# Performance work log

Hardware: AMD Instinct MI355X
Metric: run time of the kernel (lower is better)

## Reference

```python
import jax, jax.numpy as jnp
import numpy as np
import math

B, N, DIM = 4, 2048, 512
HEADS, DIM_HEAD = 8, 64
INNER = HEADS * DIM_HEAD  # 512


def setup_inputs() -> dict:
    key = jax.random.key(0)
    ks = jax.random.split(key, 4)
    x = jax.random.normal(ks[0], (B, N, DIM), dtype=jnp.float32)
    # nn.Linear(dim, inner*4, bias=False): store as [dim, 4*inner] for x @ W
    w_qkvg = jax.random.normal(ks[1], (DIM, 4 * INNER), dtype=jnp.float32) * (1.0 / math.sqrt(DIM))
    sigma = jnp.full((1, HEADS, 1, 1), 1.92, dtype=jnp.float32)
    w_out = jax.random.normal(ks[2], (2 * INNER, DIM), dtype=jnp.float32) * (1.0 / math.sqrt(2 * INNER))
    b_out = jax.random.normal(ks[3], (DIM,), dtype=jnp.float32) * 0.01
    return {"x": x, "w_qkvg": w_qkvg, "sigma": sigma, "w_out": w_out, "b_out": b_out}


def reference(x, w_qkvg, sigma, w_out, b_out):
    b, n, d = x.shape
    h, dh = HEADS, DIM_HEAD
    scale = dh ** (-0.5)

    qkvg = x @ w_qkvg  # [b, n, 4*inner]
    q, k, vg, vsigma = jnp.split(qkvg, 4, axis=-1)

    def to_heads(t):  # [b, n, h*dh] -> [b, h, n, dh]
        return t.reshape(b, n, h, dh).transpose(0, 2, 1, 3)

    q, k, vg, vsigma = map(to_heads, (q, k, vg, vsigma))

    # --- softmax branch ---
    dots = jnp.einsum('bhid,bhjd->bhij', q, k) * scale  # [b, h, n, n]
    corr_g = jax.nn.softmax(dots, axis=-1)
    out_g = jnp.matmul(corr_g, vg)  # [b, h, n, dh]

    # --- Gaussian positional-mask branch ---
    pos = jnp.arange(1, n + 1, dtype=x.dtype)
    diffs = jnp.abs(pos[:, None] - pos[None, :])  # [n, n]
    inv_norm = 1.0 / (jnp.sqrt(jnp.asarray(2.0 * math.pi, x.dtype)) * sigma)  # [1, h, 1, 1]
    gm = inv_norm * jnp.exp(-(diffs ** 2)[None, None] / (2.0 * sigma ** 2))  # [1, h, n, n]
    corr_sigma = gm / gm.sum(-1, keepdims=True)
    out_s = jnp.matmul(corr_sigma, vsigma)  # broadcasts over batch -> [b, h, n, dh]

    out = jnp.concatenate([out_g, out_s], axis=-1)  # [b, h, n, 2*dh]
    out = out.transpose(0, 2, 1, 3).reshape(b, n, 2 * h * dh)
    return out @ w_out + b_out
```

## Files before the change

### kernel.cpp

```cpp
#include <hip/hip_runtime.h>

typedef _Float16 f16;
typedef __attribute__((ext_vector_type(8))) _Float16 f16x8;
typedef __attribute__((ext_vector_type(4))) _Float16 f16x4;
typedef __attribute__((ext_vector_type(4))) float f32x4;

#define B_ 4
#define N_ 2048
#define DIM_ 512
#define H_ 8
#define DH_ 64

__device__ __forceinline__ void gload16(const void* g, void* l) {
    __builtin_amdgcn_global_load_lds((const __attribute__((address_space(1))) void*)g,
                                     (__attribute__((address_space(3))) void*)l, 16, 0, 0);
}


__global__ __launch_bounds__(256) void cvt_f16_k8(const float* __restrict__ in,
                                                  f16* __restrict__ out, int n8) {
    int i = blockIdx.x * 256 + threadIdx.x;
    if (i < n8) {
        const float4 a = ((const float4*)in)[i * 2];
        const float4 b = ((const float4*)in)[i * 2 + 1];
        f16x8 o = {(f16)a.x, (f16)a.y, (f16)a.z, (f16)a.w,
                   (f16)b.x, (f16)b.y, (f16)b.z, (f16)b.w};
        ((f16x8*)out)[i] = o;
    }
}

__global__ __launch_bounds__(256) void transpose_cvt_k(const float* __restrict__ in,
                                                       f16* __restrict__ out, int K, int N) {
    __shared__ f16 tile[64][72];
    const int nbk = K >> 6;
    const int bk = blockIdx.x % nbk, bn = blockIdx.x / nbk;
    const int k0 = bk << 6, n0 = bn << 6;
    const int t = threadIdx.x;
    const int r = t >> 2, q = (t & 3) << 4;
#pragma unroll
    for (int u = 0; u < 4; u++) {
        const float4 v = *(const float4*)&in[(size_t)(k0 + r) * N + n0 + q + u * 4];
        tile[q + u * 4 + 0][r] = (f16)v.x;
        tile[q + u * 4 + 1][r] = (f16)v.y;
        tile[q + u * 4 + 2][r] = (f16)v.z;
        tile[q + u * 4 + 3][r] = (f16)v.w;
    }
    __syncthreads();
#pragma unroll
    for (int u = 0; u < 2; u++) {
        f16x8 o = *(const f16x8*)&tile[r][q + u * 8];
        *(f16x8*)&out[(size_t)(n0 + r) * K + k0 + q + u * 8] = o;
    }
}

template <int EPI>
__global__ __launch_bounds__(256) void gemm_bt(
    const f16* __restrict__ A, const f16* __restrict__ BT, int K, int N,
    f16* __restrict__ qb, f16* __restrict__ kb, f16* __restrict__ vbT,
    float* __restrict__ vsb, const float* __restrict__ bias, float* __restrict__ outp)
{
    __shared__ char sAb[16384];
    __shared__ char sBb[16384];
    const int tid = threadIdx.x;
    const int m0 = blockIdx.y * 128, n0 = blockIdx.x * 128;
    const int wave = tid >> 6, lane = tid & 63;
    const int wr = wave >> 1, wc = wave & 1;
    const int lr = lane & 15, lg = lane >> 4;

    f32x4 acc[4][4];
    const f32x4 zero = {0.f, 0.f, 0.f, 0.f};
#pragma unroll
    for (int i = 0; i < 4; i++)
#pragma unroll
        for (int j = 0; j < 4; j++) acc[i][j] = zero;

    const f16* srcA[4]; const f16* srcB[4];
    char* ldsA[4]; char* ldsB[4];
#pragma unroll
    for (int u = 0; u < 4; u++) {
        int row = wave * 8 + u * 32 + (lane >> 3);
        int e0 = ((lane & 7) ^ (row & 7)) << 3;
        srcA[u] = A + (size_t)(m0 + row) * K + e0;
        srcB[u] = BT + (size_t)(n0 + row) * K + e0;
        ldsA[u] = sAb + wave * 1024 + u * 4096;
        ldsB[u] = sBb + wave * 1024 + u * 4096;
    }

    const int swz = (lr & 7) << 4;
    for (int kt = 0; kt < K; kt += 64) {
#pragma unroll
        for (int u = 0; u < 4; u++) {
            gload16(srcA[u], ldsA[u]);
            gload16(srcB[u], ldsB[u]);
            srcA[u] += 64; srcB[u] += 64;
        }
        __syncthreads();
#pragma unroll
        for (int half = 0; half < 2; half++) {
            f16x8 af[4], bf[4];
#pragma unroll
            for (int i = 0; i < 4; i++) {
                int R = wr * 64 + i * 16 + lr;
                af[i] = *(const f16x8*)(sAb + R * 128 + (((half << 6) | (lg << 4)) ^ swz));
            }
#pragma unroll
            for (int j = 0; j < 4; j++) {
                int R = wc * 64 + j * 16 + lr;
                bf[j] = *(const f16x8*)(sBb + R * 128 + (((half << 6) | (lg << 4)) ^ swz));
            }
#pragma unroll
            for (int i = 0; i < 4; i++)
#pragma unroll
                for (int j = 0; j < 4; j++)
                    acc[i][j] = __builtin_amdgcn_mfma_f32_16x16x32_f16(af[i], bf[j], acc[i][j], 0, 0, 0);
        }
        __syncthreads();
    }

#pragma unroll
    for (int i = 0; i < 4; i++) {
#pragma unroll
        for (int j = 0; j < 4; j++) {
            int col = n0 + wc * 64 + j * 16 + lr;
            int row0 = m0 + wr * 64 + i * 16 + lg * 4;
            if (EPI == 0) {
                int sec = col >> 9, cc = col & 511;
                int h = cc >> 6, d = cc & 63;
                int b = row0 >> 11, ns = row0 & 2047;
                if (sec == 2) {
                    f16x4 o;
#pragma unroll
                    for (int r = 0; r < 4; r++) o[r] = (f16)acc[i][j][r];
                    *(f16x4*)&vbT[((size_t)(b * H_ + h) * DH_ + d) * N_ + ns] = o;
                } else if (sec == 0) {
#pragma unroll
                    for (int r = 0; r < 4; r++)
                        qb[((size_t)(b * H_ + h) * N_ + ns + r) * DH_ + d] = (f16)(acc[i][j][r] * 0.1803368801f);
                } else if (sec == 1) {
#pragma unroll
                    for (int r = 0; r < 4; r++)
                        kb[((size_t)(b * H_ + h) * N_ + ns + r) * DH_ + d] = (f16)acc[i][j][r];
                } else {
#pragma unroll
                    for (int r = 0; r < 4; r++)
                        vsb[((size_t)(b * H_ + h) * N_ + ns + r) * DH_ + d] = acc[i][j][r];
                }
            } else {
#pragma unroll
                for (int r = 0; r < 4; r++)
                    outp[(size_t)(row0 + r) * N + col] = acc[i][j][r] + bias[col];
            }
        }
    }
}

__global__ __launch_bounds__(256) void gemm_small(
    const f16* __restrict__ A, const f16* __restrict__ BT, int K, int N,
    const float* __restrict__ bias, float* __restrict__ outp)
{
    __shared__ char sAb[8192];
    __shared__ char sBb[8192];
    const int tid = threadIdx.x;
    const int m0 = blockIdx.y * 64, n0 = blockIdx.x * 64;
    const int wave = tid >> 6, lane = tid & 63;
    const int wr = wave >> 1, wc = wave & 1;
    const int lr = lane & 15, lg = lane >> 4;

    f32x4 acc[2][2];
    const f32x4 zero = {0.f, 0.f, 0.f, 0.f};
#pragma unroll
    for (int i = 0; i < 2; i++)
#pragma unroll
        for (int j = 0; j < 2; j++) acc[i][j] = zero;

    const f16* srcA[2]; const f16* srcB[2];
    char* ldsA[2]; char* ldsB[2];
#pragma unroll
    for (int u = 0; u < 2; u++) {
        int row = wave * 8 + u * 32 + (lane >> 3);
        int e0 = ((lane & 7) ^ (row & 7)) << 3;
        srcA[u] = A + (size_t)(m0 + row) * K + e0;
        srcB[u] = BT + (size_t)(n0 + row) * K + e0;
        ldsA[u] = sAb + wave * 1024 + u * 4096;
        ldsB[u] = sBb + wave * 1024 + u * 4096;
    }

    const int swz = (lr & 7) << 4;
    for (int kt = 0; kt < K; kt += 64) {
#pragma unroll
        for (int u = 0; u < 2; u++) {
            gload16(srcA[u], ldsA[u]);
            gload16(srcB[u], ldsB[u]);
            srcA[u] += 64; srcB[u] += 64;
        }
        __syncthreads();
#pragma unroll
        for (int half = 0; half < 2; half++) {
            f16x8 af[2], bf[2];
#pragma unroll
            for (int i = 0; i < 2; i++) {
                int R = wr * 32 + i * 16 + lr;
                af[i] = *(const f16x8*)(sAb + R * 128 + (((half << 6) | (lg << 4)) ^ swz));
            }
#pragma unroll
            for (int j = 0; j < 2; j++) {
                int R = wc * 32 + j * 16 + lr;
                bf[j] = *(const f16x8*)(sBb + R * 128 + (((half << 6) | (lg << 4)) ^ swz));
            }
#pragma unroll
            for (int i = 0; i < 2; i++)
#pragma unroll
                for (int j = 0; j < 2; j++)
                    acc[i][j] = __builtin_amdgcn_mfma_f32_16x16x32_f16(af[i], bf[j], acc[i][j], 0, 0, 0);
        }
        __syncthreads();
    }

#pragma unroll
    for (int i = 0; i < 2; i++)
#pragma unroll
        for (int j = 0; j < 2; j++) {
            int col = n0 + wc * 32 + j * 16 + lr;
            int row0 = m0 + wr * 32 + i * 16 + lg * 4;
#pragma unroll
            for (int r = 0; r < 4; r++)
                outp[(size_t)(row0 + r) * N + col] = acc[i][j][r] + bias[col];
        }
}

__global__ __launch_bounds__(256) void attn_k(
    const f16* __restrict__ qb, const f16* __restrict__ kb, const f16* __restrict__ vbT,
    f16* __restrict__ cat)
{
    __shared__ char sKbf[3 * 8192];
    __shared__ char sVbf[2 * 8192];
    const int tid = threadIdx.x;
    const int bid0 = blockIdx.x;
    const int obid = (bid0 & 7) * 64 + (bid0 >> 3);
    const int bh = obid >> 4, qblk = obid & 15;
    const int b = bh >> 3, h = bh & 7;
    const int wave = tid >> 6, lane = tid & 63;
    const int lr = lane & 15, lg = lane >> 4;

    const size_t base = (size_t)bh * N_ * DH_;
    const int qrow_a = qblk * 128 + wave * 32 + lr;
    const int qrow_b = qrow_a + 16;
    const f16x8 qfa0 = *(const f16x8*)&qb[base + (size_t)qrow_a * DH_ + lg * 8];
    const f16x8 qfa1 = *(const f16x8*)&qb[base + (size_t)qrow_a * DH_ + 32 + lg * 8];
    const f16x8 qfb0 = *(const f16x8*)&qb[base + (size_t)qrow_b * DH_ + lg * 8];
    const f16x8 qfb1 = *(const f16x8*)&qb[base + (size_t)qrow_b * DH_ + 32 + lg * 8];

    const f16* kq[2]; const f16* vq[2];
#pragma unroll
    for (int u = 0; u < 2; u++) {
        int row = wave * 8 + u * 32 + (lane >> 3);
        int e0 = ((lane & 7) ^ (row & 7)) << 3;
        kq[u] = kb + base + (size_t)row * 64 + e0;
        vq[u] = vbT + base + (size_t)row * 2048 + e0;
    }
    char* const ldsKw = sKbf + wave * 1024;
    char* const ldsVw = sVbf + wave * 1024;

    f32x4 Ota[4], Otb[4], lacc_a, lacc_b;
    const f32x4 zero = {0.f, 0.f, 0.f, 0.f};
#pragma unroll
    for (int dt = 0; dt < 4; dt++) { Ota[dt] = zero; Otb[dt] = zero; }
    lacc_a = zero; lacc_b = zero;
    const f16x4 onesA = {(f16)1.f, (f16)1.f, (f16)1.f, (f16)1.f};

    const int swz = (lr & 7) << 4;

#pragma unroll
    for (int u = 0; u < 2; u++) gload16(kq[u], ldsKw + u * 4096);
#pragma unroll
    for (int u = 0; u < 2; u++) gload16(vq[u], ldsVw + u * 4096);
#pragma unroll
    for (int u = 0; u < 2; u++) gload16(kq[u] + 4096, ldsKw + 8192 + u * 4096);

    int kcur = 0;
    int kpre = 2;
    for (int t = 0; t < 32; t++) {
        __builtin_amdgcn_s_barrier();
        {
            const int vtn = (t + 1) & 31, ktn = (t + 2) & 31;
            char* vdst = ldsVw + ((t + 1) & 1) * 8192;
            char* kdst = ldsKw + kpre * 8192;
#pragma unroll
            for (int u = 0; u < 2; u++) gload16(vq[u] + vtn * 64, vdst + u * 4096);
#pragma unroll
            for (int u = 0; u < 2; u++) gload16(kq[u] + ktn * 4096, kdst + u * 4096);
        }
        asm volatile("s_waitcnt vmcnt(6)" ::: "memory");
        __builtin_amdgcn_sched_barrier(0);

        const char* Kb = sKbf + kcur * 8192;
        const char* Vb = sVbf + (t & 1) * 8192;

        f32x4 sta[4], stb[4];
        __builtin_amdgcn_s_setprio(1);
#pragma unroll
        for (int ct = 0; ct < 4; ct++) {
            int row = ct * 16 + lr;
            f16x8 kf0 = *(const f16x8*)(Kb + (((row << 7) | (lg << 4)) ^ swz));
            f16x8 kf1 = *(const f16x8*)(Kb + (((row << 7) | 64 | (lg << 4)) ^ swz));
            f32x4 sa = __builtin_amdgcn_mfma_f32_16x16x32_f16(kf0, qfa0, zero, 0, 0, 0);
            sta[ct]  = __builtin_amdgcn_mfma_f32_16x16x32_f16(kf1, qfa1, sa, 0, 0, 0);
            f32x4 sb = __builtin_amdgcn_mfma_f32_16x16x32_f16(kf0, qfb0, zero, 0, 0, 0);
            stb[ct]  = __builtin_amdgcn_mfma_f32_16x16x32_f16(kf1, qfb1, sb, 0, 0, 0);
        }
        __builtin_amdgcn_s_setprio(0);

        f16x4 ppa[4], ppb[4];
#pragma unroll
        for (int ct = 0; ct < 4; ct++)
#pragma unroll
            for (int r = 0; r < 4; r++) {
                ppa[ct][r] = (f16)__builtin_amdgcn_exp2f(sta[ct][r]);
                ppb[ct][r] = (f16)__builtin_amdgcn_exp2f(stb[ct][r]);
            }

        __builtin_amdgcn_s_setprio(1);
#pragma unroll
        for (int ct = 0; ct < 4; ct++) {
            lacc_a = __builtin_amdgcn_mfma_f32_16x16x16f16(onesA, ppa[ct], lacc_a, 0, 0, 0);
            lacc_b = __builtin_amdgcn_mfma_f32_16x16x16f16(onesA, ppb[ct], lacc_b, 0, 0, 0);
        }
#pragma unroll
        for (int dt = 0; dt < 4; dt++) {
            int row = dt * 16 + lr;
#pragma unroll
            for (int ct = 0; ct < 4; ct++) {
                f16x4 vt = *(const f16x4*)(Vb + (((row << 7) | (ct * 32) | (lg << 3)) ^ swz));
                Ota[dt] = __builtin_amdgcn_mfma_f32_16x16x16f16(vt, ppa[ct], Ota[dt], 0, 0, 0);
                Otb[dt] = __builtin_amdgcn_mfma_f32_16x16x16f16(vt, ppb[ct], Otb[dt], 0, 0, 0);
            }
        }
        __builtin_amdgcn_s_setprio(0);

        kcur = (kcur == 2) ? 0 : kcur + 1;
        kpre = (kpre == 2) ? 0 : kpre + 1;
    }

    float inv_a = 1.0f / lacc_a[0];
    float inv_b = 1.0f / lacc_b[0];
#pragma unroll
    for (int dt = 0; dt < 4; dt++) {
        f16x4 oa, ob;
#pragma unroll
        for (int r = 0; r < 4; r++) {
            oa[r] = (f16)(Ota[dt][r] * inv_a);
            ob[r] = (f16)(Otb[dt][r] * inv_b);
        }
        *(f16x4*)&cat[((size_t)(b * N_ + qrow_a)) * 1024 + h * 128 + dt * 16 + lg * 4] = oa;
        *(f16x4*)&cat[((size_t)(b * N_ + qrow_b)) * 1024 + h * 128 + dt * 16 + lg * 4] = ob;
    }
}

__global__ __launch_bounds__(256) void gauss_k(
    const float* __restrict__ vsb, const float* __restrict__ sigma, f16* __restrict__ cat)
{
    const int tid = threadIdx.x;
    const int bh = blockIdx.y, b = bh >> 3, h = bh & 7;
    const int i0 = blockIdx.x * 64;
    const int wv = tid >> 6, d = tid & 63;
    const float sig = sigma[h];
    const float c = 0.72134752f / (sig * sig);

    float wt[17];
#pragma unroll
    for (int o = 0; o <= 16; o++) wt[o] = __builtin_amdgcn_exp2f(-(float)(o * o) * c);
    float wfull = wt[0];
#pragma unroll
    for (int o = 1; o <= 16; o++) wfull += 2.f * wt[o];
    const float inv_wfull = 1.0f / wfull;

    const size_t base = (size_t)bh * N_ * DH_;
    const int r0 = i0 + wv * 16 - 16;
    float v[48];
#pragma unroll
    for (int k = 0; k < 48; k++) {
        int r = r0 + k; r = r < 0 ? 0 : (r > N_ - 1 ? N_ - 1 : r);
        v[k] = vsb[base + (size_t)r * DH_ + d];
    }

#pragma unroll
    for (int it = 0; it < 16; it++) {
        int i = i0 + wv * 16 + it;
        float acc = 0.f;
        if (i >= 16 && i <= N_ - 17) {
#pragma unroll
            for (int o = -16; o <= 16; o++)
                acc += wt[o < 0 ? -o : o] * v[16 + it + o];
            acc *= inv_wfull;
        } else {
            float ws = 0.f;
#pragma unroll
            for (int o = -16; o <= 16; o++) {
                int j = i + o;
                if (j >= 0 && j <= N_ - 1) {
                    float w = wt[o < 0 ? -o : o];
                    ws += w;
                    acc += w * v[16 + it + o];
                }
            }
            acc /= ws;
        }
        cat[((size_t)(b * N_ + i)) * 1024 + h * 128 + 64 + d] = (f16)acc;
    }
}


extern "C" void kernel_launch(void* const* d_in, const int* in_sizes, int n_in,
                              void* d_out, int out_size, void* d_ws, size_t ws_size,
                              hipStream_t stream) {
    const float* x      = (const float*)d_in[0];
    const float* w_qkvg = (const float*)d_in[1];
    const float* sigma  = (const float*)d_in[2];
    const float* w_out  = (const float*)d_in[3];
    const float* b_out  = (const float*)d_in[4];
    float* out = (float*)d_out;
    char* ws = (char*)d_ws;

    const size_t MB = 1048576;
    f16*   x16 = (f16*)(ws);
    f16*   wqT = (f16*)(ws + 8 * MB);
    f16*   woT = (f16*)(ws + 10 * MB);
    f16*   qb  = (f16*)(ws + 11 * MB);
    f16*   kb  = (f16*)(ws + 19 * MB);
    f16*   vbT = (f16*)(ws + 27 * MB);
    float* vsb = (float*)(ws + 35 * MB);
    f16*   cat = (f16*)(ws + 51 * MB);
    if (ws_size < 67 * MB) return;

    cvt_f16_k8<<<2048, 256, 0, stream>>>(x, x16, B_ * N_ * DIM_ / 8);
    transpose_cvt_k<<<256, 256, 0, stream>>>(w_qkvg, wqT, 512, 2048);
    transpose_cvt_k<<<128, 256, 0, stream>>>(w_out, woT, 1024, 512);

    gemm_bt<0><<<dim3(16, 64), 256, 0, stream>>>(x16, wqT, 512, 2048,
                                                 qb, kb, vbT, vsb, nullptr, nullptr);

    attn_k<<<512, 256, 0, stream>>>(qb, kb, vbT, cat);
    gauss_k<<<dim3(32, 32), 256, 0, stream>>>(vsb, sigma, cat);

    gemm_small<<<dim3(8, 128), 256, 0, stream>>>(cat, woT, 1024, 512, b_out, out);
}
```

Measured before the change: 134.4 us.

## Split attention key range across two blocks and merge partials; store vsigma in fp16

```diff
diff --git a/kernel.cpp b/kernel.cpp
--- a/kernel.cpp
+++ b/kernel.cpp
@@ -57,7 +57,7 @@
 __global__ __launch_bounds__(256) void gemm_bt(
     const f16* __restrict__ A, const f16* __restrict__ BT, int K, int N,
     f16* __restrict__ qb, f16* __restrict__ kb, f16* __restrict__ vbT,
-    float* __restrict__ vsb, const float* __restrict__ bias, float* __restrict__ outp)
+    f16* __restrict__ vs16, const float* __restrict__ bias, float* __restrict__ outp)
 {
     __shared__ char sAb[16384];
     __shared__ char sBb[16384];
@@ -143,7 +143,7 @@
                 } else {
 #pragma unroll
                     for (int r = 0; r < 4; r++)
-                        vsb[((size_t)(b * H_ + h) * N_ + ns + r) * DH_ + d] = acc[i][j][r];
+                        vs16[((size_t)(b * H_ + h) * N_ + ns + r) * DH_ + d] = (f16)acc[i][j][r];
                 }
             } else {
 #pragma unroll
@@ -230,15 +230,16 @@
 
 __global__ __launch_bounds__(256) void attn_k(
     const f16* __restrict__ qb, const f16* __restrict__ kb, const f16* __restrict__ vbT,
-    f16* __restrict__ cat)
+    f16* __restrict__ cat, f16* __restrict__ oaccB, float* __restrict__ lacc)
 {
     __shared__ char sKbf[3 * 8192];
     __shared__ char sVbf[2 * 8192];
     const int tid = threadIdx.x;
     const int bid0 = blockIdx.x;
-    const int obid = (bid0 & 7) * 64 + (bid0 >> 3);
-    const int bh = obid >> 4, qblk = obid & 15;
+    const int obid = (bid0 & 7) * 128 + (bid0 >> 3);
+    const int bh = obid >> 5, qblk = (obid >> 1) & 15, half = obid & 1;
     const int b = bh >> 3, h = bh & 7;
+    const int hn = half << 4;
     const int wave = tid >> 6, lane = tid & 63;
     const int lr = lane & 15, lg = lane >> 4;
 
@@ -271,24 +272,23 @@
     const int swz = (lr & 7) << 4;
 
 #pragma unroll
-    for (int u = 0; u < 2; u++) gload16(kq[u], ldsKw + u * 4096);
-#pragma unroll
-    for (int u = 0; u < 2; u++) gload16(vq[u], ldsVw + u * 4096);
-#pragma unroll
-    for (int u = 0; u < 2; u++) gload16(kq[u] + 4096, ldsKw + 8192 + u * 4096);
-
-    int kcur = 0;
-    int kpre = 2;
-    for (int t = 0; t < 32; t++) {
+    for (int u = 0; u < 2; u++) gload16(kq[u] + (size_t)hn * 4096, ldsKw + u * 4096);
+#pragma unroll
+    for (int u = 0; u < 2; u++) gload16(vq[u] + hn * 64, ldsVw + u * 4096);
+#pragma unroll
+    for (int u = 0; u < 2; u++) gload16(kq[u] + (size_t)(hn + 1) * 4096, ldsKw + 8192 + u * 4096);
+
+    int kcur = 0, kpre = 2;
+    for (int t = 0; t < 16; t++) {
         __builtin_amdgcn_s_barrier();
         {
-            const int vtn = (t + 1) & 31, ktn = (t + 2) & 31;
+            const int vtn = hn + ((t + 1) & 15), ktn = hn + ((t + 2) & 15);
             char* vdst = ldsVw + ((t + 1) & 1) * 8192;
             char* kdst = ldsKw + kpre * 8192;
 #pragma unroll
             for (int u = 0; u < 2; u++) gload16(vq[u] + vtn * 64, vdst + u * 4096);
 #pragma unroll
-            for (int u = 0; u < 2; u++) gload16(kq[u] + ktn * 4096, kdst + u * 4096);
+            for (int u = 0; u < 2; u++) gload16(kq[u] + (size_t)ktn * 4096, kdst + u * 4096);
         }
         asm volatile("s_waitcnt vmcnt(6)" ::: "memory");
         __builtin_amdgcn_sched_barrier(0);
@@ -341,23 +341,47 @@
         kpre = (kpre == 2) ? 0 : kpre + 1;
     }
 
-    float inv_a = 1.0f / lacc_a[0];
-    float inv_b = 1.0f / lacc_b[0];
 #pragma unroll
     for (int dt = 0; dt < 4; dt++) {
         f16x4 oa, ob;
 #pragma unroll
         for (int r = 0; r < 4; r++) {
-            oa[r] = (f16)(Ota[dt][r] * inv_a);
-            ob[r] = (f16)(Otb[dt][r] * inv_b);
-        }
-        *(f16x4*)&cat[((size_t)(b * N_ + qrow_a)) * 1024 + h * 128 + dt * 16 + lg * 4] = oa;
-        *(f16x4*)&cat[((size_t)(b * N_ + qrow_b)) * 1024 + h * 128 + dt * 16 + lg * 4] = ob;
-    }
+            oa[r] = (f16)Ota[dt][r];
+            ob[r] = (f16)Otb[dt][r];
+        }
+        if (half == 0) {
+            *(f16x4*)&cat[((size_t)(b * N_ + qrow_a)) * 1024 + h * 128 + dt * 16 + lg * 4] = oa;
+            *(f16x4*)&cat[((size_t)(b * N_ + qrow_b)) * 1024 + h * 128 + dt * 16 + lg * 4] = ob;
+        } else {
+            *(f16x4*)&oaccB[((size_t)(bh * N_ + qrow_a)) * 64 + dt * 16 + lg * 4] = oa;
+            *(f16x4*)&oaccB[((size_t)(bh * N_ + qrow_b)) * 64 + dt * 16 + lg * 4] = ob;
+        }
+    }
+    if (lg == 0) {
+        lacc[half * (32 * N_) + bh * N_ + qrow_a] = lacc_a[0];
+        lacc[half * (32 * N_) + bh * N_ + qrow_b] = lacc_b[0];
+    }
+}
+
+__global__ __launch_bounds__(256) void combine_k(
+    f16* __restrict__ cat, const f16* __restrict__ oaccB, const float* __restrict__ lacc)
+{
+    int gi = blockIdx.x * 256 + threadIdx.x;
+    int row = gi >> 3, c8 = gi & 7;
+    int bh = row >> 11, q = row & 2047;
+    int b = bh >> 3, h = bh & 7;
+    float inv = 1.0f / (lacc[row] + lacc[32 * N_ + row]);
+    f16* cp = &cat[((size_t)(b * N_ + q)) * 1024 + h * 128 + c8 * 8];
+    f16x8 a = *(const f16x8*)cp;
+    f16x8 o2 = *(const f16x8*)&oaccB[(size_t)row * 64 + c8 * 8];
+    f16x8 o;
+#pragma unroll
+    for (int i = 0; i < 8; i++) o[i] = (f16)(((float)a[i] + (float)o2[i]) * inv);
+    *(f16x8*)cp = o;
 }
 
 __global__ __launch_bounds__(256) void gauss_k(
-    const float* __restrict__ vsb, const float* __restrict__ sigma, f16* __restrict__ cat)
+    const f16* __restrict__ vs16, const float* __restrict__ sigma, f16* __restrict__ cat)
 {
     const int tid = threadIdx.x;
     const int bh = blockIdx.y, b = bh >> 3, h = bh & 7;
@@ -380,7 +404,7 @@
 #pragma unroll
     for (int k = 0; k < 48; k++) {
         int r = r0 + k; r = r < 0 ? 0 : (r > N_ - 1 ? N_ - 1 : r);
-        v[k] = vsb[base + (size_t)r * DH_ + d];
+        v[k] = (float)vs16[base + (size_t)r * DH_ + d];
     }
 
 #pragma unroll
@@ -422,14 +446,16 @@
     char* ws = (char*)d_ws;
 
     const size_t MB = 1048576;
-    f16*   x16 = (f16*)(ws);
-    f16*   wqT = (f16*)(ws + 8 * MB);
-    f16*   woT = (f16*)(ws + 10 * MB);
-    f16*   qb  = (f16*)(ws + 11 * MB);
-    f16*   kb  = (f16*)(ws + 19 * MB);
-    f16*   vbT = (f16*)(ws + 27 * MB);
-    float* vsb = (float*)(ws + 35 * MB);
-    f16*   cat = (f16*)(ws + 51 * MB);
+    f16*   x16  = (f16*)(ws);
+    float* lacc = (float*)(ws);
+    f16*   wqT  = (f16*)(ws + 8 * MB);
+    f16*   woT  = (f16*)(ws + 10 * MB);
+    f16*   qb   = (f16*)(ws + 11 * MB);
+    f16*   kb   = (f16*)(ws + 19 * MB);
+    f16*   vbT  = (f16*)(ws + 27 * MB);
+    f16*   vs16 = (f16*)(ws + 35 * MB);
+    f16*   cat  = (f16*)(ws + 43 * MB);
+    f16*   oaccB= (f16*)(ws + 59 * MB);
     if (ws_size < 67 * MB) return;
 
     cvt_f16_k8<<<2048, 256, 0, stream>>>(x, x16, B_ * N_ * DIM_ / 8);
@@ -437,10 +463,11 @@
     transpose_cvt_k<<<128, 256, 0, stream>>>(w_out, woT, 1024, 512);
 
     gemm_bt<0><<<dim3(16, 64), 256, 0, stream>>>(x16, wqT, 512, 2048,
-                                                 qb, kb, vbT, vsb, nullptr, nullptr);
-
-    attn_k<<<512, 256, 0, stream>>>(qb, kb, vbT, cat);
-    gauss_k<<<dim3(32, 32), 256, 0, stream>>>(vsb, sigma, cat);
+                                                 qb, kb, vbT, vs16, nullptr, nullptr);
+
+    attn_k<<<1024, 256, 0, stream>>>(qb, kb, vbT, cat, oaccB, lacc);
+    combine_k<<<2048, 256, 0, stream>>>(cat, oaccB, lacc);
+    gauss_k<<<dim3(32, 32), 256, 0, stream>>>(vs16, sigma, cat);
 
     gemm_small<<<dim3(8, 128), 256, 0, stream>>>(cat, woT, 1024, 512, b_out, out);
 }
```

Result: no change. 135.5 us (+0.9%).
